# Performance work log

Measured on AMD Instinct MI355X. Metric: run time of the kernel, lower is better.

The kernel has to match this reference:

```python
import jax, jax.numpy as jnp
import numpy as np

B, N, D_IN, D_OUT = 4, 4096, 512, 256
ALPHA = 0.2          # LeakyReLU negative slope
NEG_BIG = -9e15      # value used to mask non-edges before softmax


def setup_inputs() -> dict:
    key = jax.random.key(0)
    k_h, k_adj, k_w, k_a = jax.random.split(key, 4)
    h = jax.random.normal(k_h, (B, N, D_IN), dtype=jnp.float32)
    adj = jax.random.randint(k_adj, (N, N), 0, 2, dtype=jnp.int32)
    # xavier_uniform with gain 1.414
    lim_w = 1.414 * np.sqrt(6.0 / (D_IN + D_OUT))
    Ws = jax.random.uniform(k_w, (B, D_IN, D_OUT), jnp.float32, -lim_w, lim_w)
    lim_a = 1.414 * np.sqrt(6.0 / (2 * D_OUT + 1))
    a = jax.random.uniform(k_a, (B, 2 * D_OUT, 1), jnp.float32, -lim_a, lim_a)
    return {"h": h, "adj": adj, "Ws": Ws, "a": a}


def reference(h, adj, Ws, a):
    d_out = Ws.shape[-1]
    Wh = jnp.einsum('bni,bio->bno', h, Ws)                 # [B,N,D_OUT]
    a1 = a[:, :d_out, 0]                                    # [B,D_OUT]
    a2 = a[:, d_out:, 0]                                    # [B,D_OUT]
    e1 = jnp.einsum('bno,bo->bn', Wh, a1)                   # [B,N]
    e2 = jnp.einsum('bno,bo->bn', Wh, a2)                   # [B,N]
    e = e1[:, :, None] + e2[:, None, :]                     # [B,N,N]
    e = jnp.where(e > 0, e, ALPHA * e)                      # LeakyReLU
    scores = jnp.where(adj[None, :, :] > 0, e, NEG_BIG)     # mask non-edges
    att = jax.nn.softmax(scores, axis=-1)                   # over neighbors j
    # dropout omitted (eval mode / p irrelevant for correctness baseline)
    h_prime = jnp.einsum('bnm,bmo->bno', att, Wh)           # [B,N,D_OUT]
    return jax.nn.elu(h_prime)                              # concat=True -> elu
```

## Files before the change

kernel.cpp:

```cpp
#include <hip/hip_runtime.h>
#include <hip/hip_bf16.h>
#include <stdint.h>

#define B_    4
#define NN    4096
#define DIN   512
#define DOUT  256
#define ALPHA_ 0.2f

typedef __attribute__((ext_vector_type(8))) short short8;
typedef __attribute__((ext_vector_type(4))) float f32x4;
typedef __attribute__((ext_vector_type(2))) float f32x2;

typedef const __attribute__((address_space(1))) void gconst_void;
typedef __attribute__((address_space(3))) void lds_void;

__device__ __forceinline__ unsigned short f2bf(float x) {
    union { float f; uint32_t u; } v; v.f = x;
    uint32_t r = v.u + 0x7FFFu + ((v.u >> 16) & 1u);
    return (unsigned short)(r >> 16);
}

__global__ __launch_bounds__(256) void k_prep(const int* __restrict__ adj,
                                              const float4* __restrict__ h4,
                                              const float* __restrict__ Ws,
                                              uint32_t* __restrict__ bits,
                                              uint2* __restrict__ hb,
                                              unsigned short* __restrict__ wst) {
    const int gt = blockIdx.x * 256 + threadIdx.x;
    const int NT = 2048 * 256;
    for (int idx = gt; idx < NN * NN; idx += NT) {
        unsigned long long m = __ballot(adj[idx] > 0);
        if ((threadIdx.x & 63) == 0)
            *reinterpret_cast<unsigned long long*>(bits + ((idx >> 6) << 1)) = m;
    }
    for (int idx = gt; idx < B_ * NN * DIN / 4; idx += NT) {
        float4 v = h4[idx];
        uint2 o;
        o.x = (uint32_t)f2bf(v.x) | ((uint32_t)f2bf(v.y) << 16);
        o.y = (uint32_t)f2bf(v.z) | ((uint32_t)f2bf(v.w) << 16);
        hb[idx] = o;
    }
    for (int idx = gt; idx < B_ * DOUT * DIN; idx += NT) {
        int k = idx & (DIN - 1);
        int o = (idx >> 9) & (DOUT - 1);
        int b = idx >> 17;
        wst[idx] = f2bf(Ws[((size_t)b * DIN + k) * DOUT + o]);
    }
}

__global__ __launch_bounds__(256) void k_gemm1(const unsigned short* __restrict__ hb,
                                               const unsigned short* __restrict__ wst,
                                               const float* __restrict__ a,
                                               unsigned short* __restrict__ wht,
                                               float2* __restrict__ x1t,
                                               float* __restrict__ y1t,
                                               float* __restrict__ y2t) {
    __shared__ unsigned short Ah[64 * 64];
    __shared__ unsigned short Bw[256 * 64];
    __shared__ float e1s[64], e2s[64];
    const int tid = threadIdx.x;
    const int w = tid >> 6, lane = tid & 63;
    const int l15 = lane & 15, lhi = lane >> 4;
    const int b = blockIdx.y;
    const int n0 = blockIdx.x * 64;
    const unsigned short* hrow = hb + ((size_t)b * NN + n0) * DIN;
    const unsigned short* wrow = wst + (size_t)b * DOUT * DIN;

    if (tid < 64) { e1s[tid] = 0.f; e2s[tid] = 0.f; }

    f32x4 acc[4][4] = {};

    for (int kt = 0; kt < DIN / 64; ++kt) {
        const int k0 = kt * 64;
        #pragma unroll
        for (int it = 0; it < 2; ++it) {
            int q = it * 256 + tid;
            int row = q >> 3, c = q & 7;
            const unsigned short* src = hrow + (size_t)row * DIN + k0 + 8 * (c ^ (row & 7));
            char* dst = reinterpret_cast<char*>(Ah) + it * 4096 + w * 1024;
            __builtin_amdgcn_global_load_lds((gconst_void*)src, (lds_void*)dst, 16, 0, 0);
        }
        #pragma unroll
        for (int it = 0; it < 8; ++it) {
            int q = it * 256 + tid;
            int row = q >> 3, c = q & 7;
            const unsigned short* src = wrow + (size_t)row * DIN + k0 + 8 * (c ^ (row & 7));
            char* dst = reinterpret_cast<char*>(Bw) + it * 4096 + w * 1024;
            __builtin_amdgcn_global_load_lds((gconst_void*)src, (lds_void*)dst, 16, 0, 0);
        }
        __syncthreads();
        #pragma unroll
        for (int kk = 0; kk < 2; ++kk) {
            short8 af[4], bfr[4];
            #pragma unroll
            for (int rf = 0; rf < 4; ++rf) {
                int row = rf * 16 + l15;
                int off = row * 128 + ((kk * 64 + lhi * 16) ^ ((row & 7) << 4));
                af[rf] = *reinterpret_cast<const short8*>(reinterpret_cast<const char*>(Ah) + off);
            }
            #pragma unroll
            for (int cf = 0; cf < 4; ++cf) {
                int row = w * 64 + cf * 16 + l15;
                int off = row * 128 + ((kk * 64 + lhi * 16) ^ ((row & 7) << 4));
                bfr[cf] = *reinterpret_cast<const short8*>(reinterpret_cast<const char*>(Bw) + off);
            }
            #pragma unroll
            for (int rf = 0; rf < 4; ++rf)
                #pragma unroll
                for (int cf = 0; cf < 4; ++cf)
                    acc[rf][cf] = __builtin_amdgcn_mfma_f32_16x16x32_bf16(af[rf], bfr[cf], acc[rf][cf], 0, 0, 0);
        }
        __syncthreads();
    }
    unsigned short* wb = wht + (size_t)b * DOUT * NN;
    #pragma unroll
    for (int rf = 0; rf < 4; ++rf) {
        #pragma unroll
        for (int cf = 0; cf < 4; ++cf) {
            int d = w * 64 + cf * 16 + l15;
            int m = n0 + rf * 16 + lhi * 4;
            uint2 pk;
            pk.x = (uint32_t)f2bf(acc[rf][cf][0]) | ((uint32_t)f2bf(acc[rf][cf][1]) << 16);
            pk.y = (uint32_t)f2bf(acc[rf][cf][2]) | ((uint32_t)f2bf(acc[rf][cf][3]) << 16);
            *reinterpret_cast<uint2*>(wb + (size_t)d * NN + m) = pk;
        }
    }
    const float* ab = a + b * 2 * DOUT;
    float a1v[4], a2v[4];
    #pragma unroll
    for (int cf = 0; cf < 4; ++cf) {
        int d = w * 64 + cf * 16 + l15;
        a1v[cf] = ab[d];
        a2v[cf] = ab[DOUT + d];
    }
    #pragma unroll
    for (int rf = 0; rf < 4; ++rf) {
        #pragma unroll
        for (int j = 0; j < 4; ++j) {
            float p1 = 0.f, p2 = 0.f;
            #pragma unroll
            for (int cf = 0; cf < 4; ++cf) {
                p1 = fmaf(acc[rf][cf][j], a1v[cf], p1);
                p2 = fmaf(acc[rf][cf][j], a2v[cf], p2);
            }
            #pragma unroll
            for (int msk = 1; msk < 16; msk <<= 1) {
                p1 += __shfl_xor(p1, msk);
                p2 += __shfl_xor(p2, msk);
            }
            if (l15 == 0) {
                atomicAdd(&e1s[rf * 16 + lhi * 4 + j], p1);
                atomicAdd(&e2s[rf * 16 + lhi * 4 + j], p2);
            }
        }
    }
    __syncthreads();
    if (tid < 64) {
        float e1v = e1s[tid], e2v = e2s[tid];
        x1t[b * NN + n0 + tid] = float2{__expf(e1v), __expf(ALPHA_ * e1v)};
        y1t[b * NN + n0 + tid] = __expf(e2v);
        y2t[b * NN + n0 + tid] = __expf(ALPHA_ * e2v);
    }
}

__global__ __launch_bounds__(256, 2) void k_attn(const unsigned short* __restrict__ wht,
                                                 const uint32_t* __restrict__ bits,
                                                 const float2* __restrict__ x1t,
                                                 const float* __restrict__ y1t,
                                                 const float* __restrict__ y2t,
                                                 float* __restrict__ out,
                                                 float* __restrict__ part1,
                                                 float* __restrict__ sums0,
                                                 float* __restrict__ sums1) {
    __shared__ unsigned short Bw[2 * 256 * 64];
    __shared__ unsigned short Pt[2 * 64 * 64];

    const int tid = threadIdx.x;
    const int w = tid >> 6, lane = tid & 63;
    const int l15 = lane & 15, lh4 = lane >> 4;

    const int bid = blockIdx.x;
    const int wg = ((bid & 7) << 6) | (bid >> 3);
    const int g  = wg >> 6;
    const int b  = g >> 1;
    const int n0 = ((g & 1) * 32 + (wg & 31)) << 6;
    const int T0 = ((wg >> 5) & 1) * 32;

    const int pr = tid >> 2, pc = tid & 3;
    const float2 xv = x1t[b * NN + n0 + pr];
    const float X1 = xv.x, X2 = xv.y;
    const unsigned short* wb = wht + (size_t)b * DOUT * NN;

    f32x4 acc[4][4] = {};
    f32x2 psum2 = {0.f, 0.f};

    const unsigned short* sp[8];
    #pragma unroll
    for (int it = 0; it < 8; ++it) {
        int q = it * 256 + tid;
        int row = q >> 3, c = q & 7;
        sp[it] = wb + (size_t)row * NN + T0 * 64 + 8 * (c ^ (row & 7));
    }
    const uint8_t* bp = reinterpret_cast<const uint8_t*>(bits) +
                        (size_t)(n0 + pr) * (NN / 8) + T0 * 8 + pc * 2;
    const float4* y1p = reinterpret_cast<const float4*>(y1t + b * NN + T0 * 64 + pc * 16);
    const float4* y2p = reinterpret_cast<const float4*>(y2t + b * NN + T0 * 64 + pc * 16);

#define STAGE(BUF)                                                                     \
    {                                                                                  \
        _Pragma("unroll")                                                              \
        for (int it = 0; it < 8; ++it) {                                               \
            char* dst = reinterpret_cast<char*>(Bw) + (BUF) * 32768 + it * 4096 + w * 1024; \
            __builtin_amdgcn_global_load_lds((gconst_void*)sp[it], (lds_void*)dst, 16, 0, 0); \
            sp[it] += 64;                                                              \
        }                                                                              \
    }

#define P_MATH(BB, PKW)                                                                \
    {                                                                                  \
        float4 a0 = y1p[0], a1 = y1p[1], a2 = y1p[2], a3 = y1p[3]; y1p += 16;          \
        float4 c0v = y2p[0], c1v = y2p[1], c2v = y2p[2], c3v = y2p[3]; y2p += 16;      \
        float v1[16] = {a0.x, a0.y, a0.z, a0.w, a1.x, a1.y, a1.z, a1.w,                \
                        a2.x, a2.y, a2.z, a2.w, a3.x, a3.y, a3.z, a3.w};               \
        float v2[16] = {c0v.x, c0v.y, c0v.z, c0v.w, c1v.x, c1v.y, c1v.z, c1v.w,        \
                        c2v.x, c2v.y, c2v.z, c2v.w, c3v.x, c3v.y, c3v.z, c3v.w};       \
        _Pragma("unroll")                                                              \
        for (int i = 0; i < 8; ++i) {                                                  \
            f32x2 pa = f32x2{v1[2 * i], v1[2 * i + 1]} * X1;                           \
            f32x2 pb = f32x2{v2[2 * i], v2[2 * i + 1]} * X2;                           \
            f32x2 pm = __builtin_elementwise_max(pa, pb);                              \
            union { __hip_bfloat162 h; uint32_t u; } cc;                               \
            cc.h = __float22bfloat162_rn(float2{pm.x, pm.y});                          \
            uint32_t b2 = ((BB) >> (2 * i)) & 3u;                                      \
            uint32_t mk = ((b2 & 1u) ? 0xFFFFu : 0u) | ((b2 & 2u) ? 0xFFFF0000u : 0u); \
            uint32_t q = cc.u & mk;                                                    \
            PKW[i] = q;                                                                \
            union { uint32_t u; float f; } qlo, qhi;                                   \
            qlo.u = q << 16; qhi.u = q & 0xFFFF0000u;                                  \
            psum2 += f32x2{qlo.f, qhi.f};                                              \
        }                                                                              \
    }

#define PT_WRITE(PKW, BUF)                                                             \
    {                                                                                  \
        uint4 qa; qa.x = PKW[0]; qa.y = PKW[1]; qa.z = PKW[2]; qa.w = PKW[3];          \
        uint4 qb; qb.x = PKW[4]; qb.y = PKW[5]; qb.z = PKW[6]; qb.w = PKW[7];          \
        char* base = reinterpret_cast<char*>(Pt) + (BUF) * 8192 + pr * 128;            \
        *reinterpret_cast<uint4*>(base + ((pc * 32)      ^ ((pr & 7) << 4))) = qa;     \
        *reinterpret_cast<uint4*>(base + ((pc * 32 + 16) ^ ((pr & 7) << 4))) = qb;     \
    }

#define MM(CUR)                                                                        \
    {                                                                                  \
        const char* bwb = reinterpret_cast<const char*>(Bw) + (CUR) * 32768;           \
        const char* ptb = reinterpret_cast<const char*>(Pt) + (CUR) * 8192;            \
        __builtin_amdgcn_s_setprio(1);                                                 \
        _Pragma("unroll")                                                              \
        for (int kk = 0; kk < 2; ++kk) {                                               \
            short8 af[4];                                                              \
            _Pragma("unroll")                                                          \
            for (int rf = 0; rf < 4; ++rf) {                                           \
                int row = rf * 16 + l15;                                               \
                int off = row * 128 + ((kk * 64 + lh4 * 16) ^ ((row & 7) << 4));       \
                af[rf] = *reinterpret_cast<const short8*>(ptb + off);                  \
            }                                                                          \
            _Pragma("unroll")                                                          \
            for (int cf = 0; cf < 4; ++cf) {                                           \
                int row = w * 64 + cf * 16 + l15;                                      \
                int off = row * 128 + ((kk * 64 + lh4 * 16) ^ ((row & 7) << 4));       \
                short8 bf = *reinterpret_cast<const short8*>(bwb + off);               \
                _Pragma("unroll")                                                      \
                for (int rf = 0; rf < 4; ++rf)                                         \
                    acc[rf][cf] = __builtin_amdgcn_mfma_f32_16x16x32_bf16(             \
                        af[rf], bf, acc[rf][cf], 0, 0, 0);                             \
            }                                                                          \
        }                                                                              \
        __builtin_amdgcn_s_setprio(0);                                                 \
    }

    STAGE(0)
    {
        uint32_t bb = *reinterpret_cast<const uint16_t*>(bp); bp += 8;
        uint32_t pkw[8];
        P_MATH(bb, pkw)
        PT_WRITE(pkw, 0)
    }
    __syncthreads();

    for (int t = 0; t < 32; ++t) {
        const int cur = t & 1;
        if (t < 31) {
            STAGE(cur ^ 1)
            uint32_t bb = *reinterpret_cast<const uint16_t*>(bp); bp += 8;
            uint32_t pkw[8];
            P_MATH(bb, pkw)
            PT_WRITE(pkw, cur ^ 1)
        }
        MM(cur)
        __syncthreads();
    }
#undef STAGE
#undef P_MATH
#undef PT_WRITE
#undef MM

    float ps = psum2.x + psum2.y;
    ps += __shfl_xor(ps, 1);
    ps += __shfl_xor(ps, 2);
    if (pc == 0) {
        float* sdst = (T0 == 0) ? sums0 : sums1;
        sdst[b * NN + n0 + pr] = ps;
    }

    float* pdst = (T0 == 0) ? out : part1;
    #pragma unroll
    for (int rf = 0; rf < 4; ++rf) {
        #pragma unroll
        for (int cf = 0; cf < 4; ++cf) {
            int d = w * 64 + cf * 16 + l15;
            #pragma unroll
            for (int j = 0; j < 4; ++j) {
                int nr = n0 + rf * 16 + lh4 * 4 + j;
                pdst[((size_t)b * NN + nr) * DOUT + d] = acc[rf][cf][j];
            }
        }
    }
}

__global__ __launch_bounds__(256) void k_final(const float* __restrict__ part1,
                                               const float* __restrict__ sums0,
                                               const float* __restrict__ sums1,
                                               float* __restrict__ out) {
    int f4 = blockIdx.x * 256 + threadIdx.x;
    int row = f4 >> 6;
    float inv = 1.0f / (sums0[row] + sums1[row]);
    float4 v = reinterpret_cast<const float4*>(out)[f4];
    float4 p = reinterpret_cast<const float4*>(part1)[f4];
    v.x = (v.x + p.x) * inv;
    v.y = (v.y + p.y) * inv;
    v.z = (v.z + p.z) * inv;
    v.w = (v.w + p.w) * inv;
    v.x = v.x > 0.f ? v.x : (__expf(v.x) - 1.f);
    v.y = v.y > 0.f ? v.y : (__expf(v.y) - 1.f);
    v.z = v.z > 0.f ? v.z : (__expf(v.z) - 1.f);
    v.w = v.w > 0.f ? v.w : (__expf(v.w) - 1.f);
    reinterpret_cast<float4*>(out)[f4] = v;
}

extern "C" void kernel_launch(void* const* d_in, const int* in_sizes, int n_in,
                              void* d_out, int out_size, void* d_ws, size_t ws_size,
                              hipStream_t stream) {
    (void)in_sizes; (void)n_in; (void)out_size; (void)ws_size;
    const float* h   = (const float*)d_in[0];
    const int*   adj = (const int*)d_in[1];
    const float* Ws  = (const float*)d_in[2];
    const float* a   = (const float*)d_in[3];
    float* out = (float*)d_out;

    char* ws = (char*)d_ws;
    unsigned short* hb  = (unsigned short*)(ws);
    unsigned short* wst = (unsigned short*)(ws + 16777216);
    unsigned short* wht = (unsigned short*)(ws + 17825792);
    float2* x1t = (float2*)(ws + 26214400);
    float*  y1t = (float*)(ws + 26345472);
    float*  y2t = (float*)(ws + 26411008);
    uint32_t* bits = (uint32_t*)(ws + 26476544);
    float* sums0 = (float*)(ws + 28573696);
    float* sums1 = (float*)(ws + 28639232);
    float* part1 = (float*)hb;

    k_prep<<<dim3(2048), dim3(256), 0, stream>>>(adj, (const float4*)h, Ws,
                                                 bits, (uint2*)hb, wst);
    k_gemm1<<<dim3(NN / 64, B_), dim3(256), 0, stream>>>(hb, wst, a, wht, x1t, y1t, y2t);
    k_attn<<<dim3(512), dim3(256), 0, stream>>>(wht, bits, x1t, y1t, y2t,
                                                out, part1, sums0, sums1);
    k_final<<<dim3(B_ * NN * DOUT / 1024), dim3(256), 0, stream>>>(part1, sums0, sums1, out);
}
```

Baseline: 114.0 us.

## Load Wh B-fragments directly into registers instead of staging through LDS

Removes the LDS buffer for the Wh tile. Each lane now loads its MFMA B-operand fragments straight from global memory into registers, double-buffered across two register sets, and the loop is unrolled by two so the buffers alternate. This cuts LDS capacity and LDS read traffic and may allow higher occupancy. In exchange it uses more VGPRs and issues less coalesced global loads, since each lane reads 16-byte chunks from separate rows.

```diff
diff --git a/kernel.cpp b/kernel.cpp
--- a/kernel.cpp
+++ b/kernel.cpp
@@ -173,7 +173,6 @@
                                                  float* __restrict__ part1,
                                                  float* __restrict__ sums0,
                                                  float* __restrict__ sums1) {
-    __shared__ unsigned short Bw[2 * 256 * 64];
     __shared__ unsigned short Pt[2 * 64 * 64];
 
     const int tid = threadIdx.x;
@@ -195,25 +194,23 @@
     f32x4 acc[4][4] = {};
     f32x2 psum2 = {0.f, 0.f};
 
-    const unsigned short* sp[8];
-    #pragma unroll
-    for (int it = 0; it < 8; ++it) {
-        int q = it * 256 + tid;
-        int row = q >> 3, c = q & 7;
-        sp[it] = wb + (size_t)row * NN + T0 * 64 + 8 * (c ^ (row & 7));
-    }
+    const unsigned short* bptr[4];
+    #pragma unroll
+    for (int cf = 0; cf < 4; ++cf)
+        bptr[cf] = wb + (size_t)(w * 64 + cf * 16 + l15) * NN + T0 * 64 + lh4 * 8;
+
     const uint8_t* bp = reinterpret_cast<const uint8_t*>(bits) +
                         (size_t)(n0 + pr) * (NN / 8) + T0 * 8 + pc * 2;
     const float4* y1p = reinterpret_cast<const float4*>(y1t + b * NN + T0 * 64 + pc * 16);
     const float4* y2p = reinterpret_cast<const float4*>(y2t + b * NN + T0 * 64 + pc * 16);
 
-#define STAGE(BUF)                                                                     \
+#define BLOAD(REGS)                                                                    \
     {                                                                                  \
         _Pragma("unroll")                                                              \
-        for (int it = 0; it < 8; ++it) {                                               \
-            char* dst = reinterpret_cast<char*>(Bw) + (BUF) * 32768 + it * 4096 + w * 1024; \
-            __builtin_amdgcn_global_load_lds((gconst_void*)sp[it], (lds_void*)dst, 16, 0, 0); \
-            sp[it] += 64;                                                              \
+        for (int cf = 0; cf < 4; ++cf) {                                               \
+            REGS[cf * 2]     = *reinterpret_cast<const short8*>(bptr[cf]);             \
+            REGS[cf * 2 + 1] = *reinterpret_cast<const short8*>(bptr[cf] + 32);        \
+            bptr[cf] += 64;                                                            \
         }                                                                              \
     }
 
@@ -251,10 +248,9 @@
         *reinterpret_cast<uint4*>(base + ((pc * 32 + 16) ^ ((pr & 7) << 4))) = qb;     \
     }
 
-#define MM(CUR)                                                                        \
+#define MM(BUF, REGS)                                                                  \
     {                                                                                  \
-        const char* bwb = reinterpret_cast<const char*>(Bw) + (CUR) * 32768;           \
-        const char* ptb = reinterpret_cast<const char*>(Pt) + (CUR) * 8192;            \
+        const char* ptb = reinterpret_cast<const char*>(Pt) + (BUF) * 8192;            \
         __builtin_amdgcn_s_setprio(1);                                                 \
         _Pragma("unroll")                                                              \
         for (int kk = 0; kk < 2; ++kk) {                                               \
@@ -266,20 +262,18 @@
                 af[rf] = *reinterpret_cast<const short8*>(ptb + off);                  \
             }                                                                          \
             _Pragma("unroll")                                                          \
-            for (int cf = 0; cf < 4; ++cf) {                                           \
-                int row = w * 64 + cf * 16 + l15;                                      \
-                int off = row * 128 + ((kk * 64 + lh4 * 16) ^ ((row & 7) << 4));       \
-                short8 bf = *reinterpret_cast<const short8*>(bwb + off);               \
+            for (int cf = 0; cf < 4; ++cf)                                             \
                 _Pragma("unroll")                                                      \
                 for (int rf = 0; rf < 4; ++rf)                                         \
                     acc[rf][cf] = __builtin_amdgcn_mfma_f32_16x16x32_bf16(             \
-                        af[rf], bf, acc[rf][cf], 0, 0, 0);                             \
-            }                                                                          \
+                        af[rf], REGS[cf * 2 + kk], acc[rf][cf], 0, 0, 0);              \
         }                                                                              \
         __builtin_amdgcn_s_setprio(0);                                                 \
     }
 
-    STAGE(0)
+    short8 bfA[8], bfB[8];
+
+    BLOAD(bfA)
     {
         uint32_t bb = *reinterpret_cast<const uint16_t*>(bp); bp += 8;
         uint32_t pkw[8];
@@ -288,19 +282,27 @@
     }
     __syncthreads();
 
-    for (int t = 0; t < 32; ++t) {
-        const int cur = t & 1;
-        if (t < 31) {
-            STAGE(cur ^ 1)
+    for (int t = 0; t < 32; t += 2) {
+        {
+            BLOAD(bfB)
             uint32_t bb = *reinterpret_cast<const uint16_t*>(bp); bp += 8;
             uint32_t pkw[8];
             P_MATH(bb, pkw)
-            PT_WRITE(pkw, cur ^ 1)
-        }
-        MM(cur)
+            PT_WRITE(pkw, 1)
+        }
+        MM(0, bfA)
         __syncthreads();
-    }
-#undef STAGE
+        if (t + 2 < 32) {
+            BLOAD(bfA)
+            uint32_t bb = *reinterpret_cast<const uint16_t*>(bp); bp += 8;
+            uint32_t pkw[8];
+            P_MATH(bb, pkw)
+            PT_WRITE(pkw, 0)
+        }
+        MM(1, bfB)
+        __syncthreads();
+    }
+#undef BLOAD
 #undef P_MATH
 #undef PT_WRITE
 #undef MM
```

New measurement: 147.7 us. 1.3x slower.
